# Kernel optimization log

Measured on AMD Instinct MI355X. Metric: run time of the kernel, lower is better.

Reference implementation:

```python
import jax, jax.numpy as jnp
import numpy as np

VOCAB = 8192
CTX = 4  # sum(context_length) = sum((2,2))
BATCH = 1024


def setup_inputs() -> dict:
    key = jax.random.key(0)
    k1, k2, k3 = jax.random.split(key, 3)
    contexts = jax.random.randint(k1, (BATCH, CTX), 0, VOCAB, dtype=jnp.int64 if jax.config.read('jax_enable_x64') else jnp.int32)
    # torch Linear(in=CTX*VOCAB, out=VOCAB): weight [VOCAB, CTX*VOCAB], bias [VOCAB]
    fc_w = jax.random.normal(k2, (VOCAB, CTX * VOCAB), dtype=jnp.float32) * 0.02
    fc_b = jax.random.normal(k3, (VOCAB,), dtype=jnp.float32) * 0.02
    return {"contexts": contexts, "fc_w": fc_w, "fc_b": fc_b}


def reference(contexts, fc_w, fc_b):
    # out[b, o] = sum_{i,v} onehot(contexts)[b,i,v] * fc_w[o, i*V + v] + fc_b[o]
    #           = sum_i fc_w[o, i*V + contexts[b,i]] + fc_b[o]
    # i.e. the dense one-hot GEMM is a row-gather over the fc weight.
    V = fc_b.shape[0]
    B, C = contexts.shape
    # [C, V_in, V_out]
    w = fc_w.reshape(V, C, V).transpose(1, 2, 0)
    pos = jnp.arange(C)[None, :]          # [1, C]
    gathered = w[pos, contexts]           # [B, C, V_out]
    return gathered.sum(axis=1) + fc_b    # [B, V_out]
```

## Files before the change

### kernel.cpp

```cpp
#include <hip/hip_runtime.h>

#define VOCAB 8192
#define CTX 4
#define BATCH 1024
#define OBLK 16
#define NCHUNK (OBLK * CTX)

__global__ __launch_bounds__(1024) void cbow_kernel(
    const int*   __restrict__ contexts,
    const float* __restrict__ fc_w,
    const float* __restrict__ fc_b,
    float*       __restrict__ out)
{
    __shared__ float lds[2][VOCAB];

    const int t  = threadIdx.x;
    const int o0 = blockIdx.x * OBLK;
    const size_t base = (size_t)o0 * (CTX * VOCAB);

    const int4 cv = ((const int4*)contexts)[t];
    const int cc[4] = {cv.x, cv.y, cv.z, cv.w};

    float acc[OBLK];
#pragma unroll
    for (int j = 0; j < OBLK; ++j) acc[j] = fc_b[o0 + j];

    {
        const float4* src = (const float4*)(fc_w + base);
        float4 a  = src[t];
        float4 b2 = src[1024 + t];
        float4* dst = (float4*)lds[0];
        dst[t]        = a;
        dst[1024 + t] = b2;
    }
    __syncthreads();

#pragma unroll
    for (int k = 0; k < NCHUNK; ++k) {
        float4 a, b2;
        if (k < NCHUNK - 1) {
            const float4* src = (const float4*)(fc_w + base + (size_t)(k + 1) * VOCAB);
            a  = src[t];
            b2 = src[1024 + t];
        }

        acc[k >> 2] += lds[k & 1][cc[k & 3]];

        if (k < NCHUNK - 1) {
            float4* dst = (float4*)lds[(k + 1) & 1];
            dst[t]        = a;
            dst[1024 + t] = b2;
        }
        __syncthreads();
    }

    float4* op = (float4*)(out + (size_t)t * VOCAB + o0);
#pragma unroll
    for (int j = 0; j < OBLK / 4; ++j) {
        float4 v;
        v.x = acc[4 * j + 0];
        v.y = acc[4 * j + 1];
        v.z = acc[4 * j + 2];
        v.w = acc[4 * j + 3];
        op[j] = v;
    }
}

extern "C" void kernel_launch(void* const* d_in, const int* in_sizes, int n_in,
                              void* d_out, int out_size, void* d_ws, size_t ws_size,
                              hipStream_t stream) {
    const int*   contexts = (const int*)d_in[0];
    const float* fc_w     = (const float*)d_in[1];
    const float* fc_b     = (const float*)d_in[2];
    float*       out      = (float*)d_out;

    dim3 grid(VOCAB / OBLK);
    dim3 block(1024);
    cbow_kernel<<<grid, block, 0, stream>>>(contexts, fc_w, fc_b, out);
}
```

Measured before the change: 206.3 us.

## Replace LDS-staged weight streaming with direct global gathers per context

Removes the double-buffered LDS staging of full weight rows and the per-chunk barriers. Each thread now gathers its four context columns directly from global memory for each of the 16 output rows. This drops the streaming of the whole 1 GiB weight matrix and reads only the touched elements. The cost is scattered, uncoalesced 4-byte global loads with sector over-fetch. A min-blocks hint is also added to launch bounds.

Measured after the change: 484.2 us. 135% more time.

```diff
diff --git a/kernel.cpp b/kernel.cpp
--- a/kernel.cpp
+++ b/kernel.cpp
@@ -2,56 +2,32 @@
 
 #define VOCAB 8192
 #define CTX 4
-#define BATCH 1024
 #define OBLK 16
-#define NCHUNK (OBLK * CTX)
+#define ROWSTRIDE (CTX * VOCAB)
 
-__global__ __launch_bounds__(1024) void cbow_kernel(
+__global__ __launch_bounds__(1024, 8) void cbow_kernel(
     const int*   __restrict__ contexts,
     const float* __restrict__ fc_w,
     const float* __restrict__ fc_b,
     float*       __restrict__ out)
 {
-    __shared__ float lds[2][VOCAB];
-
     const int t  = threadIdx.x;
     const int o0 = blockIdx.x * OBLK;
-    const size_t base = (size_t)o0 * (CTX * VOCAB);
 
     const int4 cv = ((const int4*)contexts)[t];
-    const int cc[4] = {cv.x, cv.y, cv.z, cv.w};
+    const int col0 = 0 * VOCAB + cv.x;
+    const int col1 = 1 * VOCAB + cv.y;
+    const int col2 = 2 * VOCAB + cv.z;
+    const int col3 = 3 * VOCAB + cv.w;
 
     float acc[OBLK];
 #pragma unroll
     for (int j = 0; j < OBLK; ++j) acc[j] = fc_b[o0 + j];
 
-    {
-        const float4* src = (const float4*)(fc_w + base);
-        float4 a  = src[t];
-        float4 b2 = src[1024 + t];
-        float4* dst = (float4*)lds[0];
-        dst[t]        = a;
-        dst[1024 + t] = b2;
-    }
-    __syncthreads();
-
 #pragma unroll
-    for (int k = 0; k < NCHUNK; ++k) {
-        float4 a, b2;
-        if (k < NCHUNK - 1) {
-            const float4* src = (const float4*)(fc_w + base + (size_t)(k + 1) * VOCAB);
-            a  = src[t];
-            b2 = src[1024 + t];
-        }
-
-        acc[k >> 2] += lds[k & 1][cc[k & 3]];
-
-        if (k < NCHUNK - 1) {
-            float4* dst = (float4*)lds[(k + 1) & 1];
-            dst[t]        = a;
-            dst[1024 + t] = b2;
-        }
-        __syncthreads();
+    for (int j = 0; j < OBLK; ++j) {
+        const float* row = fc_w + (size_t)(o0 + j) * ROWSTRIDE;
+        acc[j] += (row[col0] + row[col1]) + (row[col2] + row[col3]);
     }
 
     float4* op = (float4*)(out + (size_t)t * VOCAB + o0);
```
